# Performance work log

Measured on AMD Instinct MI355X. Metric: run time of the kernel, lower is better.

The kernel has to match this reference:

```python
import jax, jax.numpy as jnp
import numpy as np

NUM_HEADS = 16


def setup_inputs() -> dict:
    key = jax.random.key(0)
    ks = jax.random.split(key, 5)
    B, S, D = 2, 2048, 1024
    scale = 0.02
    return {
        "x": jax.random.normal(ks[0], (B, S, D), dtype=jnp.float32),
        "Wq": jax.random.normal(ks[1], (D, D), dtype=jnp.float32) * scale,
        "Wk": jax.random.normal(ks[2], (D, D), dtype=jnp.float32) * scale,
        "Wv": jax.random.normal(ks[3], (D, D), dtype=jnp.float32) * scale,
        "Wo": jax.random.normal(ks[4], (D, D), dtype=jnp.float32) * scale,
        "bo": jnp.zeros((D,), dtype=jnp.float32),
    }


def reference(x, Wq, Wk, Wv, Wo, bo):
    B, S, D = x.shape
    H = NUM_HEADS
    Dh = D // H
    # project and split heads -> [B, H, S, Dh]
    q = (x @ Wq).reshape(B, S, H, Dh).transpose(0, 2, 1, 3)
    k = (x @ Wk).reshape(B, S, H, Dh).transpose(0, 2, 1, 3)
    v = (x @ Wv).reshape(B, S, H, Dh).transpose(0, 2, 1, 3)
    # full causal attention scores [B, H, S, S]
    scores = jnp.einsum("bhqd,bhkd->bhqk", q, k)
    causal_mask = jnp.triu(jnp.ones((S, S), dtype=bool), k=1)
    scores = jnp.where(causal_mask, -jnp.inf, scores)
    attn = jax.nn.softmax(scores / jnp.sqrt(jnp.float32(Dh)), axis=-1)
    ctx = jnp.einsum("bhqk,bhkd->bhqd", attn, v)
    ctx = ctx.transpose(0, 2, 1, 3).reshape(B, S, D)
    return ctx @ Wo + bo
```

## Files before the change

### kernel.cpp

```cpp
#include <hip/hip_runtime.h>
#include <hip/hip_bf16.h>
#include <math.h>

typedef __bf16 bf16_t;
typedef bf16_t bf16x4 __attribute__((ext_vector_type(4)));
typedef bf16_t bf16x8 __attribute__((ext_vector_type(8)));
typedef float f32x4 __attribute__((ext_vector_type(4)));
typedef unsigned int u32;
typedef u32 u32x2 __attribute__((ext_vector_type(2)));
typedef u32 u32x4 __attribute__((ext_vector_type(4)));

#define MFMA16(a, b, c) __builtin_amdgcn_mfma_f32_16x16x32_bf16(a, b, c, 0, 0, 0)
#define NEG_BIG (-1e30f)
#define QSCALE 0.18033688f

#define GLL16(gp, lp)                                                          \
    __builtin_amdgcn_global_load_lds(                                          \
        (const __attribute__((address_space(1))) unsigned int*)(gp),           \
        (__attribute__((address_space(3))) unsigned int*)(lp), 16, 0, 0)


__global__ __launch_bounds__(256) void prep(const float* __restrict__ x,
                                            const float* __restrict__ Wq,
                                            const float* __restrict__ Wk,
                                            const float* __restrict__ Wv,
                                            const float* __restrict__ Wo,
                                            bf16_t* __restrict__ Xb,
                                            bf16_t* __restrict__ WTqkv,
                                            bf16_t* __restrict__ WoT) {
    __shared__ float tile[32][33];
    const int z = blockIdx.z;
    const int tx = threadIdx.x, ty = threadIdx.y;
    if (z == 4) {
        int i0 = (((blockIdx.y * 32 + blockIdx.x) * 256) + ty * 32 + tx) * 4;
        for (int j = 0; j < 4; j++) {
            int i = i0 + j * 1048576;
            float4 v = *(const float4*)(x + i);
            Xb[i + 0] = (bf16_t)v.x;
            Xb[i + 1] = (bf16_t)v.y;
            Xb[i + 2] = (bf16_t)v.z;
            Xb[i + 3] = (bf16_t)v.w;
        }
    } else {
        const float* W = (z == 0) ? Wq : (z == 1) ? Wk : (z == 2) ? Wv : Wo;
        bf16_t* WT = (z < 3) ? (WTqkv + (size_t)z * 1048576) : WoT;
        int bx = blockIdx.x * 32, by = blockIdx.y * 32;
        for (int i = 0; i < 32; i += 8)
            tile[ty + i][tx] = W[(size_t)(by + ty + i) * 1024 + bx + tx];
        __syncthreads();
        for (int i = 0; i < 32; i += 8)
            WT[(size_t)(bx + ty + i) * 1024 + by + tx] = (bf16_t)tile[tx][ty + i];
    }
}

__global__ __launch_bounds__(256) void gemm_qkv(const bf16_t* __restrict__ X,
                                                const bf16_t* __restrict__ WT,
                                                bf16_t* __restrict__ Qd,
                                                bf16_t* __restrict__ Kd,
                                                bf16_t* __restrict__ Vd) {
    __shared__ bf16_t AsmF[2][128 * 64];
    __shared__ bf16_t BsmF[2][128 * 64];
    const int bid = blockIdx.x;
    const int logical = (bid & 7) * 96 + (bid >> 3);
    const int which = logical >> 8;
    const int rem = logical & 255;
    const bf16_t* Wt = WT + (size_t)which * 1024 * 1024;
    const int bm = (rem >> 3) * 128;
    const int bn = (rem & 7) * 128;
    const int tid = threadIdx.x;
    const int wave = tid >> 6, lane = tid & 63;
    const int wm = (wave >> 1) * 64, wn = (wave & 1) * 64;
    const int col = lane & 15, quad = lane >> 4;
    const int cswz = col & 7;
    const int lr8 = lane >> 3;
    const int jg = (lane & 7) ^ lr8;

    const int srow = wave * 32 + lr8;
    const bf16_t* gA = X  + (size_t)(bm + srow) * 1024 + jg * 8;
    const bf16_t* gB = Wt + (size_t)(bn + srow) * 1024 + jg * 8;

    auto stage = [&](int k0, int bsel) {
        bf16_t* lA = AsmF[bsel] + wave * 2048;
        bf16_t* lB = BsmF[bsel] + wave * 2048;
        for (int j = 0; j < 4; j++) {
            GLL16(gA + (size_t)j * 8192 + k0, lA + j * 512);
            GLL16(gB + (size_t)j * 8192 + k0, lB + j * 512);
        }
    };

    stage(0, 0);

    f32x4 acc[4][4] = {};

    for (int t = 0; t < 16; t++) {
        __syncthreads();
        if (t + 1 < 16) stage((t + 1) * 64, (t + 1) & 1);
        const bf16_t* Ab = AsmF[t & 1];
        const bf16_t* Bb = BsmF[t & 1];
        for (int ks = 0; ks < 2; ks++) {
            bf16x8 af[4], bfr[4];
            for (int mi = 0; mi < 4; mi++)
                af[mi] = *(const bf16x8*)&Ab[(wm + mi * 16 + col) * 64 +
                                             (((ks << 2) + quad) ^ cswz) * 8];
            for (int ni = 0; ni < 4; ni++)
                bfr[ni] = *(const bf16x8*)&Bb[(wn + ni * 16 + col) * 64 +
                                              (((ks << 2) + quad) ^ cswz) * 8];
            if (which != 2) {
                for (int mi = 0; mi < 4; mi++)
                    for (int ni = 0; ni < 4; ni++)
                        acc[mi][ni] = MFMA16(af[mi], bfr[ni], acc[mi][ni]);
            } else {
                for (int mi = 0; mi < 4; mi++)
                    for (int ni = 0; ni < 4; ni++)
                        acc[mi][ni] = MFMA16(bfr[ni], af[mi], acc[mi][ni]);
            }
        }
    }

    if (which != 2) {
        const float sc = (which == 0) ? QSCALE : 1.0f;
        for (int mi = 0; mi < 4; mi++) {
            for (int ni = 0; ni < 4; ni++) {
                int mbase = bm + wm + mi * 16 + quad * 4;
                int n = bn + wn + ni * 16 + col;
                int h = n >> 6, dh = n & 63;
                for (int r = 0; r < 4; r++) {
                    int m = mbase + r;
                    int b = m >> 11, s = m & 2047;
                    size_t bh = (size_t)b * 16 + h;
                    bf16_t val = (bf16_t)(acc[mi][ni][r] * sc);
                    if (which == 0) Qd[(bh * 2048 + s) * 64 + dh] = val;
                    else            Kd[(bh * 2048 + s) * 64 + dh] = val;
                }
            }
        }
    } else {
        for (int mi = 0; mi < 4; mi++) {
            for (int ni = 0; ni < 4; ni++) {
                int nbase = bn + wn + ni * 16 + quad * 4;
                int m = bm + wm + mi * 16 + col;
                int b = m >> 11, s = m & 2047;
                for (int r = 0; r < 4; r++) {
                    int n = nbase + r;
                    int h = n >> 6, dh = n & 63;
                    size_t bh = (size_t)b * 16 + h;
                    Vd[(bh * 64 + dh) * 2048 + s] = (bf16_t)acc[mi][ni][r];
                }
            }
        }
    }
}

__global__ __launch_bounds__(256) void attn(const bf16_t* __restrict__ Q,
                                            const bf16_t* __restrict__ K,
                                            const bf16_t* __restrict__ VT,
                                            bf16_t* __restrict__ CTX) {
    __shared__ bf16_t KsF[2 * 64 * 64];
    __shared__ bf16_t VsF[2 * 64 * 64];

    const int bidx = blockIdx.x;
    const int bh = bidx & 31;
    const int qt = 31 - (bidx >> 5);
    const int tid = threadIdx.x;
    const int wave = tid >> 6, lane = tid & 63;
    const int col = lane & 15, quad = lane >> 4;
    const int cswz = col & 7;
    const int lr8 = lane >> 3;
    const int jg = (lane & 7) ^ lr8;

    const bf16_t* Qb = Q + (size_t)bh * 2048 * 64;
    const bf16_t* Kb = K + (size_t)bh * 2048 * 64;
    const bf16_t* Vb = VT + (size_t)bh * 64 * 2048;

    const int strow = wave * 16 + lr8;
    const bf16_t* gK = Kb + (size_t)strow * 64 + jg * 8;
    const bf16_t* gV = Vb + (size_t)strow * 2048 + jg * 8;

    const int b_ = bh >> 4, h_ = bh & 15;

    bf16x8 ones;
    for (int i = 0; i < 8; i++) ones[i] = (bf16_t)1.0f;

    auto stage = [&](int k0, int bsel) {
        bf16_t* lK = KsF + bsel * 4096 + wave * 1024;
        bf16_t* lV = VsF + bsel * 4096 + wave * 1024;
        for (int j = 0; j < 2; j++) {
            GLL16(gK + (size_t)(k0 + j * 8) * 64, lK + j * 512);
            GLL16(gV + (size_t)(k0 + j * 8 * 2048), lV + j * 512);
        }
    };

    stage(0, 0);

    const int q0 = qt * 64;
    const int qrow = q0 + wave * 16 + col;
    const bf16x8 qf0 = *(const bf16x8*)&Qb[(size_t)qrow * 64 + quad * 8];
    const bf16x8 qf1 = *(const bf16x8*)&Qb[(size_t)qrow * 64 + 32 + quad * 8];

    f32x4 o[4] = {};
    f32x4 accl = {};

    const int iA = (col | ((quad & 1) << 5)) << 2;
    const bool hi = (quad & 2) != 0;

    const int nt = qt + 1;
    for (int g = 0; g < nt; g++) {
        __syncthreads();
        if (g + 1 < nt) stage((g + 1) * 64, (g + 1) & 1);

        const int bsel = g & 1;
        const bf16_t* Kbuf = KsF + bsel * 4096;
        const bf16_t* Vbuf = VsF + bsel * 4096;
        const bool diag = (g == qt);

        u32x2 pwd[4];
#pragma unroll
        for (int ksub = 0; ksub < 4; ksub++) {
            bf16x8 a0 = *(const bf16x8*)&Kbuf[(ksub * 16 + col) * 64 +
                                              (quad ^ cswz) * 8];
            bf16x8 a1 = *(const bf16x8*)&Kbuf[(ksub * 16 + col) * 64 +
                                              ((4 + quad) ^ cswz) * 8];
            f32x4 z = {};
            z = MFMA16(a0, qf0, z);
            z = MFMA16(a1, qf1, z);
            if (diag) {
                for (int r = 0; r < 4; r++) {
                    int lk = ksub * 16 + quad * 4 + r;
                    if (lk > wave * 16 + col) z[r] = NEG_BIG;
                }
            }
            bf16x4 pw;
#pragma unroll
            for (int r = 0; r < 4; r++)
                pw[r] = (bf16_t)__builtin_amdgcn_exp2f(z[r]);
            pwd[ksub] = __builtin_bit_cast(u32x2, pw);
        }

#pragma unroll
        for (int ck = 0; ck < 2; ck++) {
            u32x2 sA = pwd[2 * ck], sB = pwd[2 * ck + 1];
            int w0a = __builtin_amdgcn_ds_bpermute(iA,      (int)sA.x);
            int w0b = __builtin_amdgcn_ds_bpermute(iA,      (int)sB.x);
            int w1a = __builtin_amdgcn_ds_bpermute(iA,      (int)sA.y);
            int w1b = __builtin_amdgcn_ds_bpermute(iA,      (int)sB.y);
            int w2a = __builtin_amdgcn_ds_bpermute(iA + 64, (int)sA.x);
            int w2b = __builtin_amdgcn_ds_bpermute(iA + 64, (int)sB.x);
            int w3a = __builtin_amdgcn_ds_bpermute(iA + 64, (int)sA.y);
            int w3b = __builtin_amdgcn_ds_bpermute(iA + 64, (int)sB.y);
            u32x4 pu = {(u32)(hi ? w0b : w0a), (u32)(hi ? w1b : w1a),
                        (u32)(hi ? w2b : w2a), (u32)(hi ? w3b : w3a)};
            bf16x8 pf = __builtin_bit_cast(bf16x8, pu);

            accl = MFMA16(pf, ones, accl);
            for (int d = 0; d < 4; d++) {
                bf16x8 vf = *(const bf16x8*)&Vbuf[(d * 16 + col) * 64 +
                                                  (((ck << 2) + quad) ^ cswz) * 8];
                o[d] = MFMA16(pf, vf, o[d]);
            }
        }
    }

    for (int r = 0; r < 4; r++) {
        float rl = __builtin_amdgcn_rcpf(fmaxf(accl[r], 1e-20f));
        int s = q0 + wave * 16 + quad * 4 + r;
        for (int d = 0; d < 4; d++) {
            CTX[((size_t)(b_ * 2048 + s)) * 1024 + h_ * 64 + d * 16 + col] =
                (bf16_t)(o[d][r] * rl);
        }
    }
}

__global__ __launch_bounds__(256) void gemm_out(const bf16_t* __restrict__ X,
                                                const bf16_t* __restrict__ WT,
                                                const float* __restrict__ BO,
                                                float* __restrict__ OUT) {
    __shared__ bf16_t AsmF[2][64 * 64];
    __shared__ bf16_t BsmF[2][128 * 64];
    const int bid = blockIdx.x;
    const int logical = (bid & 7) * 64 + (bid >> 3);
    const int bm = (logical >> 3) * 64;
    const int bn = (logical & 7) * 128;
    const int tid = threadIdx.x;
    const int wave = tid >> 6, lane = tid & 63;
    const int wm = (wave >> 1) * 32, wn = (wave & 1) * 64;
    const int col = lane & 15, quad = lane >> 4;
    const int cswz = col & 7;
    const int lr8 = lane >> 3;
    const int jg = (lane & 7) ^ lr8;

    const int arow = wave * 16 + lr8;
    const int brow = wave * 32 + lr8;
    const bf16_t* gA = X  + (size_t)(bm + arow) * 1024 + jg * 8;
    const bf16_t* gB = WT + (size_t)(bn + brow) * 1024 + jg * 8;

    auto stage = [&](int k0, int bsel) {
        bf16_t* lA = AsmF[bsel] + wave * 1024;
        bf16_t* lB = BsmF[bsel] + wave * 2048;
        for (int j = 0; j < 2; j++)
            GLL16(gA + (size_t)j * 8192 + k0, lA + j * 512);
        for (int j = 0; j < 4; j++)
            GLL16(gB + (size_t)j * 8192 + k0, lB + j * 512);
    };

    stage(0, 0);

    f32x4 acc[2][4] = {};

    for (int t = 0; t < 16; t++) {
        __syncthreads();
        if (t + 1 < 16) stage((t + 1) * 64, (t + 1) & 1);
        const bf16_t* Ab = AsmF[t & 1];
        const bf16_t* Bb = BsmF[t & 1];
        for (int ks = 0; ks < 2; ks++) {
            bf16x8 af[2], bfr[4];
            for (int mi = 0; mi < 2; mi++)
                af[mi] = *(const bf16x8*)&Ab[(wm + mi * 16 + col) * 64 +
                                             (((ks << 2) + quad) ^ cswz) * 8];
            for (int ni = 0; ni < 4; ni++)
                bfr[ni] = *(const bf16x8*)&Bb[(wn + ni * 16 + col) * 64 +
                                              (((ks << 2) + quad) ^ cswz) * 8];
            for (int mi = 0; mi < 2; mi++)
                for (int ni = 0; ni < 4; ni++)
                    acc[mi][ni] = MFMA16(af[mi], bfr[ni], acc[mi][ni]);
        }
    }

    for (int mi = 0; mi < 2; mi++) {
        for (int ni = 0; ni < 4; ni++) {
            int mbase = bm + wm + mi * 16 + quad * 4;
            int n = bn + wn + ni * 16 + col;
            float bov = BO[n];
            for (int r = 0; r < 4; r++) {
                int m = mbase + r;
                OUT[(size_t)m * 1024 + n] = acc[mi][ni][r] + bov;
            }
        }
    }
}

extern "C" void kernel_launch(void* const* d_in, const int* in_sizes, int n_in,
                              void* d_out, int out_size, void* d_ws, size_t ws_size,
                              hipStream_t stream) {
    const float* x  = (const float*)d_in[0];
    const float* Wq = (const float*)d_in[1];
    const float* Wk = (const float*)d_in[2];
    const float* Wv = (const float*)d_in[3];
    const float* Wo = (const float*)d_in[4];
    const float* bo = (const float*)d_in[5];
    float* out = (float*)d_out;

    const size_t MEG = 1048576;
    bf16_t* base  = (bf16_t*)d_ws;
    bf16_t* Xb    = base;
    bf16_t* WTqkv = base + 4 * MEG;
    bf16_t* WoT   = base + 7 * MEG;
    bf16_t* Qb    = base + 8 * MEG;
    bf16_t* Kb    = base + 12 * MEG;
    bf16_t* Vb    = base + 16 * MEG;
    bf16_t* Cb    = base + 20 * MEG;

    prep<<<dim3(32, 32, 5), dim3(32, 8), 0, stream>>>(x, Wq, Wk, Wv, Wo,
                                                      Xb, WTqkv, WoT);
    gemm_qkv<<<768, 256, 0, stream>>>(Xb, WTqkv, Qb, Kb, Vb);
    attn<<<1024, 256, 0, stream>>>(Qb, Kb, Vb, Cb);
    gemm_out<<<512, 256, 0, stream>>>(Cb, WoT, bo, out);
}
```

Before: 183.2 us.

## Give each attention wave two query row groups and single-buffer output GEMM

```diff
diff --git a/kernel.cpp b/kernel.cpp
--- a/kernel.cpp
+++ b/kernel.cpp
@@ -151,7 +151,7 @@
     }
 }
 
-__global__ __launch_bounds__(256) void attn(const bf16_t* __restrict__ Q,
+__global__ __launch_bounds__(128) void attn(const bf16_t* __restrict__ Q,
                                             const bf16_t* __restrict__ K,
                                             const bf16_t* __restrict__ VT,
                                             bf16_t* __restrict__ CTX) {
@@ -172,7 +172,7 @@
     const bf16_t* Kb = K + (size_t)bh * 2048 * 64;
     const bf16_t* Vb = VT + (size_t)bh * 64 * 2048;
 
-    const int strow = wave * 16 + lr8;
+    const int strow = wave * 32 + lr8;
     const bf16_t* gK = Kb + (size_t)strow * 64 + jg * 8;
     const bf16_t* gV = Vb + (size_t)strow * 2048 + jg * 8;
 
@@ -182,9 +182,9 @@
     for (int i = 0; i < 8; i++) ones[i] = (bf16_t)1.0f;
 
     auto stage = [&](int k0, int bsel) {
-        bf16_t* lK = KsF + bsel * 4096 + wave * 1024;
-        bf16_t* lV = VsF + bsel * 4096 + wave * 1024;
-        for (int j = 0; j < 2; j++) {
+        bf16_t* lK = KsF + bsel * 4096 + wave * 2048;
+        bf16_t* lV = VsF + bsel * 4096 + wave * 2048;
+        for (int j = 0; j < 4; j++) {
             GLL16(gK + (size_t)(k0 + j * 8) * 64, lK + j * 512);
             GLL16(gV + (size_t)(k0 + j * 8 * 2048), lV + j * 512);
         }
@@ -193,12 +193,14 @@
     stage(0, 0);
 
     const int q0 = qt * 64;
-    const int qrow = q0 + wave * 16 + col;
-    const bf16x8 qf0 = *(const bf16x8*)&Qb[(size_t)qrow * 64 + quad * 8];
-    const bf16x8 qf1 = *(const bf16x8*)&Qb[(size_t)qrow * 64 + 32 + quad * 8];
-
-    f32x4 o[4] = {};
-    f32x4 accl = {};
+    const int qrA = q0 + wave * 32 + col;
+    const bf16x8 qfA0 = *(const bf16x8*)&Qb[(size_t)qrA * 64 + quad * 8];
+    const bf16x8 qfA1 = *(const bf16x8*)&Qb[(size_t)qrA * 64 + 32 + quad * 8];
+    const bf16x8 qfB0 = *(const bf16x8*)&Qb[(size_t)(qrA + 16) * 64 + quad * 8];
+    const bf16x8 qfB1 = *(const bf16x8*)&Qb[(size_t)(qrA + 16) * 64 + 32 + quad * 8];
+
+    f32x4 o[2][4] = {};
+    f32x4 accl[2] = {};
 
     const int iA = (col | ((quad & 1) << 5)) << 2;
     const bool hi = (quad & 2) != 0;
@@ -213,59 +215,71 @@
         const bf16_t* Vbuf = VsF + bsel * 4096;
         const bool diag = (g == qt);
 
-        u32x2 pwd[4];
+        u32x2 pwd[2][4];
 #pragma unroll
         for (int ksub = 0; ksub < 4; ksub++) {
             bf16x8 a0 = *(const bf16x8*)&Kbuf[(ksub * 16 + col) * 64 +
                                               (quad ^ cswz) * 8];
             bf16x8 a1 = *(const bf16x8*)&Kbuf[(ksub * 16 + col) * 64 +
                                               ((4 + quad) ^ cswz) * 8];
-            f32x4 z = {};
-            z = MFMA16(a0, qf0, z);
-            z = MFMA16(a1, qf1, z);
-            if (diag) {
-                for (int r = 0; r < 4; r++) {
-                    int lk = ksub * 16 + quad * 4 + r;
-                    if (lk > wave * 16 + col) z[r] = NEG_BIG;
+#pragma unroll
+            for (int G = 0; G < 2; G++) {
+                f32x4 z = {};
+                z = MFMA16(a0, G ? qfB0 : qfA0, z);
+                z = MFMA16(a1, G ? qfB1 : qfA1, z);
+                if (diag) {
+                    int qloc = wave * 32 + G * 16 + col;
+                    for (int r = 0; r < 4; r++) {
+                        int lk = ksub * 16 + quad * 4 + r;
+                        if (lk > qloc) z[r] = NEG_BIG;
+                    }
                 }
-            }
-            bf16x4 pw;
-#pragma unroll
-            for (int r = 0; r < 4; r++)
-                pw[r] = (bf16_t)__builtin_amdgcn_exp2f(z[r]);
-            pwd[ksub] = __builtin_bit_cast(u32x2, pw);
+                bf16x4 pw;
+#pragma unroll
+                for (int r = 0; r < 4; r++)
+                    pw[r] = (bf16_t)__builtin_amdgcn_exp2f(z[r]);
+                pwd[G][ksub] = __builtin_bit_cast(u32x2, pw);
+            }
         }
 
 #pragma unroll
         for (int ck = 0; ck < 2; ck++) {
-            u32x2 sA = pwd[2 * ck], sB = pwd[2 * ck + 1];
-            int w0a = __builtin_amdgcn_ds_bpermute(iA,      (int)sA.x);
-            int w0b = __builtin_amdgcn_ds_bpermute(iA,      (int)sB.x);
-            int w1a = __builtin_amdgcn_ds_bpermute(iA,      (int)sA.y);
-            int w1b = __builtin_amdgcn_ds_bpermute(iA,      (int)sB.y);
-            int w2a = __builtin_amdgcn_ds_bpermute(iA + 64, (int)sA.x);
-            int w2b = __builtin_amdgcn_ds_bpermute(iA + 64, (int)sB.x);
-            int w3a = __builtin_amdgcn_ds_bpermute(iA + 64, (int)sA.y);
-            int w3b = __builtin_amdgcn_ds_bpermute(iA + 64, (int)sB.y);
-            u32x4 pu = {(u32)(hi ? w0b : w0a), (u32)(hi ? w1b : w1a),
-                        (u32)(hi ? w2b : w2a), (u32)(hi ? w3b : w3a)};
-            bf16x8 pf = __builtin_bit_cast(bf16x8, pu);
-
-            accl = MFMA16(pf, ones, accl);
+            bf16x8 vf[4];
+#pragma unroll
+            for (int d = 0; d < 4; d++)
+                vf[d] = *(const bf16x8*)&Vbuf[(d * 16 + col) * 64 +
+                                              (((ck << 2) + quad) ^ cswz) * 8];
+#pragma unroll
+            for (int G = 0; G < 2; G++) {
+                u32x2 sA = pwd[G][2 * ck], sB = pwd[G][2 * ck + 1];
+                int w0a = __builtin_amdgcn_ds_bpermute(iA,      (int)sA.x);
+                int w0b = __builtin_amdgcn_ds_bpermute(iA,      (int)sB.x);
+                int w1a = __builtin_amdgcn_ds_bpermute(iA,      (int)sA.y);
+                int w1b = __builtin_amdgcn_ds_bpermute(iA,      (int)sB.y);
+                int w2a = __builtin_amdgcn_ds_bpermute(iA + 64, (int)sA.x);
+                int w2b = __builtin_amdgcn_ds_bpermute(iA + 64, (int)sB.x);
+                int w3a = __builtin_amdgcn_ds_bpermute(iA + 64, (int)sA.y);
+                int w3b = __builtin_amdgcn_ds_bpermute(iA + 64, (int)sB.y);
+                u32x4 pu = {(u32)(hi ? w0b : w0a), (u32)(hi ? w1b : w1a),
+                            (u32)(hi ? w2b : w2a), (u32)(hi ? w3b : w3a)};
+                bf16x8 pf = __builtin_bit_cast(bf16x8, pu);
+
+                accl[G] = MFMA16(pf, ones, accl[G]);
+                for (int d = 0; d < 4; d++)
+                    o[G][d] = MFMA16(pf, vf[d], o[G][d]);
+            }
+        }
+    }
+
+#pragma unroll
+    for (int G = 0; G < 2; G++) {
+        for (int r = 0; r < 4; r++) {
+            float rl = __builtin_amdgcn_rcpf(fmaxf(accl[G][r], 1e-20f));
+            int s = q0 + wave * 32 + G * 16 + quad * 4 + r;
             for (int d = 0; d < 4; d++) {
-                bf16x8 vf = *(const bf16x8*)&Vbuf[(d * 16 + col) * 64 +
-                                                  (((ck << 2) + quad) ^ cswz) * 8];
-                o[d] = MFMA16(pf, vf, o[d]);
-            }
-        }
-    }
-
-    for (int r = 0; r < 4; r++) {
-        float rl = __builtin_amdgcn_rcpf(fmaxf(accl[r], 1e-20f));
-        int s = q0 + wave * 16 + quad * 4 + r;
-        for (int d = 0; d < 4; d++) {
-            CTX[((size_t)(b_ * 2048 + s)) * 1024 + h_ * 64 + d * 16 + col] =
-                (bf16_t)(o[d][r] * rl);
+                CTX[((size_t)(b_ * 2048 + s)) * 1024 + h_ * 64 + d * 16 + col] =
+                    (bf16_t)(o[G][d][r] * rl);
+            }
         }
     }
 }
@@ -274,8 +288,8 @@
                                                 const bf16_t* __restrict__ WT,
                                                 const float* __restrict__ BO,
                                                 float* __restrict__ OUT) {
-    __shared__ bf16_t AsmF[2][64 * 64];
-    __shared__ bf16_t BsmF[2][128 * 64];
+    __shared__ bf16_t AsmF[64 * 64];
+    __shared__ bf16_t BsmF[128 * 64];
     const int bid = blockIdx.x;
     const int logical = (bid & 7) * 64 + (bid >> 3);
     const int bm = (logical >> 3) * 64;
@@ -292,37 +306,30 @@
     const int brow = wave * 32 + lr8;
     const bf16_t* gA = X  + (size_t)(bm + arow) * 1024 + jg * 8;
     const bf16_t* gB = WT + (size_t)(bn + brow) * 1024 + jg * 8;
-
-    auto stage = [&](int k0, int bsel) {
-        bf16_t* lA = AsmF[bsel] + wave * 1024;
-        bf16_t* lB = BsmF[bsel] + wave * 2048;
+    bf16_t* lA = AsmF + wave * 1024;
+    bf16_t* lB = BsmF + wave * 2048;
+
+    f32x4 acc[2][4] = {};
+
+    for (int k0 = 0; k0 < 1024; k0 += 64) {
         for (int j = 0; j < 2; j++)
             GLL16(gA + (size_t)j * 8192 + k0, lA + j * 512);
         for (int j = 0; j < 4; j++)
             GLL16(gB + (size_t)j * 8192 + k0, lB + j * 512);
-    };
-
-    stage(0, 0);
-
-    f32x4 acc[2][4] = {};
-
-    for (int t = 0; t < 16; t++) {
-        __syncthreads();
-        if (t + 1 < 16) stage((t + 1) * 64, (t + 1) & 1);
-        const bf16_t* Ab = AsmF[t & 1];
-        const bf16_t* Bb = BsmF[t & 1];
+        __syncthreads();
         for (int ks = 0; ks < 2; ks++) {
             bf16x8 af[2], bfr[4];
             for (int mi = 0; mi < 2; mi++)
-                af[mi] = *(const bf16x8*)&Ab[(wm + mi * 16 + col) * 64 +
-                                             (((ks << 2) + quad) ^ cswz) * 8];
+                af[mi] = *(const bf16x8*)&AsmF[(wm + mi * 16 + col) * 64 +
+                                               (((ks << 2) + quad) ^ cswz) * 8];
             for (int ni = 0; ni < 4; ni++)
-                bfr[ni] = *(const bf16x8*)&Bb[(wn + ni * 16 + col) * 64 +
-                                              (((ks << 2) + quad) ^ cswz) * 8];
+                bfr[ni] = *(const bf16x8*)&BsmF[(wn + ni * 16 + col) * 64 +
+                                                (((ks << 2) + quad) ^ cswz) * 8];
             for (int mi = 0; mi < 2; mi++)
                 for (int ni = 0; ni < 4; ni++)
                     acc[mi][ni] = MFMA16(af[mi], bfr[ni], acc[mi][ni]);
         }
+        __syncthreads();
     }
 
     for (int mi = 0; mi < 2; mi++) {
@@ -362,6 +369,6 @@
     prep<<<dim3(32, 32, 5), dim3(32, 8), 0, stream>>>(x, Wq, Wk, Wv, Wo,
                                                       Xb, WTqkv, WoT);
     gemm_qkv<<<768, 256, 0, stream>>>(Xb, WTqkv, Qb, Kb, Vb);
-    attn<<<1024, 256, 0, stream>>>(Qb, Kb, Vb, Cb);
+    attn<<<1024, 128, 0, stream>>>(Qb, Kb, Vb, Cb);
     gemm_out<<<512, 256, 0, stream>>>(Cb, WoT, bo, out);
 }
```

Measured after the change: 183.5 us. About the same (+0.2%).
